# Optimization experiments

Hardware: AMD Instinct MI355X
Metric: run time of the kernel (lower is better)

The kernel has to match this reference:

```python
import jax, jax.numpy as jnp
import numpy as np

N, IN_DIM, OUT_DIM, HEADS = 2048, 512, 512, 8
HEAD_DIM = OUT_DIM // HEADS
NEG_SLOPE = 0.2


def setup_inputs() -> dict:
    key = jax.random.key(0)
    k1, k2, k3, k4 = jax.random.split(key, 4)
    x = jax.random.normal(k1, (N, IN_DIM), dtype=jnp.float32)
    adj = jax.random.randint(k2, (N, N), 0, 2, dtype=jnp.int32)
    W = jax.random.normal(k3, (IN_DIM, OUT_DIM), dtype=jnp.float32) * 0.02
    a = jax.random.normal(k4, (2 * HEAD_DIM,), dtype=jnp.float32) * 0.02
    return {"x": x, "adj": adj, "W": W, "a": a}


def reference(x, adj, W, a):
    # Wh: (N, H, Dh)
    Wh = (x @ W).reshape(N, HEADS, HEAD_DIM)
    # a . concat(Wh_i, Wh_j) == (Wh_i . a_src) + (Wh_j . a_dst) -- exact decomposition,
    # avoids materializing the (N, N, H, 2*Dh) concat tensor.
    a_src, a_dst = a[:HEAD_DIM], a[HEAD_DIM:]
    s_i = jnp.einsum('nhd,d->nh', Wh, a_src)  # contribution of dest node i
    s_j = jnp.einsum('nhd,d->nh', Wh, a_dst)  # contribution of source node j
    e = jax.nn.leaky_relu(s_i[:, None, :] + s_j[None, :, :], negative_slope=NEG_SLOPE)  # (N, N, H)
    mask = (adj > 0)[:, :, None]
    e = jnp.where(mask, e, jnp.float32(-jnp.inf))
    alpha = jax.nn.softmax(e, axis=1)  # softmax over source nodes j
    # out[i,h,:] = sum_j alpha[i,j,h] * Wh[j,h,:]   (dropout is identity at eval)
    out = jnp.einsum('ijh,jhd->ihd', alpha, Wh)
    return out.reshape(N, OUT_DIM)
```

## Files before the change

kernel.cpp:

```cpp
#include <hip/hip_runtime.h>
#include <hip/hip_bf16.h>

#define NN 2048
#define KD 512
#define ODIM 512
#define NHEAD 8
#define HD 64
#define NEG 0.2f

typedef float f32x4 __attribute__((ext_vector_type(4)));
typedef short bf16x8 __attribute__((ext_vector_type(8)));
typedef short bf16x4 __attribute__((ext_vector_type(4)));
typedef unsigned long long u64;
typedef unsigned int u32;

__device__ __forceinline__ short tob(float f) {
  __hip_bfloat16 h = __float2bfloat16(f);
  return *reinterpret_cast<short*>(&h);
}

__device__ __forceinline__ void gl_lds16(const void* g, void* l) {
  __builtin_amdgcn_global_load_lds(
      (const __attribute__((address_space(1))) u32*)g,
      (__attribute__((address_space(3))) u32*)l, 16, 0, 0);
}

__global__ __launch_bounds__(256) void prep(const float* __restrict__ W,
                                            const int* __restrict__ adj,
                                            __hip_bfloat16* __restrict__ WTb,
                                            unsigned short* __restrict__ bits) {
  const int b = blockIdx.x;
  const int t = threadIdx.x;
  if (b >= 64) {
    const int T = (b - 64) * 256 + t;
    const int row = T >> 7, g = T & 127;
    const int* p = adj + (size_t)row * NN + g * 16;
    u32 m = 0;
#pragma unroll
    for (int q = 0; q < 4; ++q) {
      const int4 v = *(const int4*)&p[q * 4];
      m |= (v.x > 0 ? 1u : 0u) << (q * 4);
      m |= (v.y > 0 ? 2u : 0u) << (q * 4);
      m |= (v.z > 0 ? 4u : 0u) << (q * 4);
      m |= (v.w > 0 ? 8u : 0u) << (q * 4);
    }
    bits[T] = (unsigned short)m;
    return;
  }
  __shared__ float tile[64][68];
  const int k0 = (b & 7) * 64, od0 = (b >> 3) * 64;
#pragma unroll
  for (int r = 0; r < 4; ++r) {
    const int flat = r * 256 + t;
    const int kk = flat >> 4, oq = (flat & 15) * 4;
    const float4 v = *(const float4*)&W[(size_t)(k0 + kk) * ODIM + od0 + oq];
    tile[kk][oq] = v.x;
    tile[kk][oq + 1] = v.y;
    tile[kk][oq + 2] = v.z;
    tile[kk][oq + 3] = v.w;
  }
  __syncthreads();
#pragma unroll
  for (int r = 0; r < 2; ++r) {
    const int flat = r * 256 + t;
    const int od = flat >> 3, kq = (flat & 7) * 8;
    bf16x8 o;
#pragma unroll
    for (int u = 0; u < 8; ++u) o[u] = tob(tile[kq + u][od]);
    *(bf16x8*)&WTb[(size_t)(od0 + od) * KD + k0 + kq] = o;
  }
}

__global__ __launch_bounds__(256) void gemm_fused(
    const float* __restrict__ X, const __hip_bfloat16* __restrict__ WTb,
    const float* __restrict__ a, short* __restrict__ WhF,
    float2* __restrict__ esrcp, u32* __restrict__ edstp) {
  __shared__ short As[64][72];
  __shared__ short Bs[64][72];
  const int t = threadIdx.x;
  const int lane = t & 63, w = t >> 6;
  const int col = lane & 15, kgrp = lane >> 4;
  const int bm = blockIdx.x * 64;
  const int h = blockIdx.y;

  const int am = t >> 2, ak = (t & 3) * 16;
  const int bn = t >> 2, bk = (t & 3) * 16;

  float4 xa[4];
  bf16x8 wb[2];
#pragma unroll
  for (int q = 0; q < 4; ++q)
    xa[q] = *(const float4*)&X[(size_t)(bm + am) * KD + ak + q * 4];
#pragma unroll
  for (int q = 0; q < 2; ++q)
    wb[q] = *(const bf16x8*)&WTb[(size_t)(h * 64 + bn) * KD + bk + q * 8];

  f32x4 acc[4] = {};

  for (int k0 = 0; k0 < KD; k0 += 64) {
#pragma unroll
    for (int q = 0; q < 2; ++q) {
      bf16x8 o;
#pragma unroll
      for (int u = 0; u < 4; ++u) {
        o[u] = tob(((const float*)&xa[q * 2])[u]);
        o[u + 4] = tob(((const float*)&xa[q * 2 + 1])[u]);
      }
      *(bf16x8*)&As[am][ak + q * 8] = o;
      *(bf16x8*)&Bs[bn][bk + q * 8] = wb[q];
    }
    __syncthreads();
    if (k0 + 64 < KD) {
      const int k1 = k0 + 64;
#pragma unroll
      for (int q = 0; q < 4; ++q)
        xa[q] = *(const float4*)&X[(size_t)(bm + am) * KD + k1 + ak + q * 4];
#pragma unroll
      for (int q = 0; q < 2; ++q)
        wb[q] = *(const bf16x8*)&WTb[(size_t)(h * 64 + bn) * KD + k1 + bk + q * 8];
    }
#pragma unroll
    for (int ks = 0; ks < 2; ++ks) {
      const bf16x8 af = *(const bf16x8*)&As[w * 16 + col][ks * 32 + kgrp * 8];
#pragma unroll
      for (int nt = 0; nt < 4; ++nt) {
        const bf16x8 bf = *(const bf16x8*)&Bs[nt * 16 + col][ks * 32 + kgrp * 8];
        acc[nt] = __builtin_amdgcn_mfma_f32_16x16x32_bf16(af, bf, acc[nt], 0, 0, 0);
      }
    }
    __syncthreads();
  }

  float asv[4], adv[4];
#pragma unroll
  for (int nt = 0; nt < 4; ++nt) {
    asv[nt] = a[nt * 16 + col];
    adv[nt] = a[64 + nt * 16 + col];
  }
  float ps[4], pd[4];
#pragma unroll
  for (int r = 0; r < 4; ++r) {
    float s1 = 0.f, s2 = 0.f;
#pragma unroll
    for (int nt = 0; nt < 4; ++nt) {
      s1 += acc[nt][r] * asv[nt];
      s2 += acc[nt][r] * adv[nt];
    }
    ps[r] = s1;
    pd[r] = s2;
  }
#pragma unroll
  for (int off = 1; off <= 8; off <<= 1) {
#pragma unroll
    for (int r = 0; r < 4; ++r) {
      ps[r] += __shfl_xor(ps[r], off);
      pd[r] += __shfl_xor(pd[r], off);
    }
  }
  {
    const size_t tbase = ((size_t)h * 32 + blockIdx.x) * 4096;
    const int lp = ((w & 1) * 2 + (kgrp >> 1)) * 16 + col;
    const int u0 = (kgrp & 1) * 4;
    const int slot_ks = w >> 1;
#pragma unroll
    for (int nt = 0; nt < 4; ++nt) {
      bf16x4 o;
#pragma unroll
      for (int r = 0; r < 4; ++r) o[r] = tob(acc[nt][r]);
      *(bf16x4*)&WhF[tbase + (size_t)(nt * 2 + slot_ks) * 512 + lp * 8 + u0] = o;
    }
  }
  if (col == 0) {
    const int mbase = bm + w * 16 + kgrp * 4;
#pragma unroll
    for (int r = 0; r < 4; ++r) {
      const int n = mbase + r;
      esrcp[h * NN + n] = make_float2(__expf(ps[r]), __expf(NEG * ps[r]));
      const u32 lo = (u32)(unsigned short)tob(__expf(pd[r]));
      const u32 hi = (u32)(unsigned short)tob(__expf(NEG * pd[r]));
      edstp[h * NN + n] = (hi << 16) | lo;
    }
  }
}

__global__ __launch_bounds__(256) void attn_mfma(
    const short* __restrict__ WhF, const unsigned char* __restrict__ adjbits,
    const float2* __restrict__ esrcp, const u32* __restrict__ edstp,
    float* __restrict__ out) {
  extern __shared__ __align__(16) char smem[];
  const int t = threadIdx.x;
  const int lane = t & 63;
  const int jq = t >> 6;
  const int col = lane & 15, kgrp = lane >> 4;
  const int h = blockIdx.y;
  const int i0 = blockIdx.x * 32;

  const short* tb = WhF + ((size_t)h * 32 + jq * 8) * 4096;
  const int jb = jq * 512;

  const float2 e0 = esrcp[h * NN + i0 + col];
  const float2 e1 = esrcp[h * NN + i0 + 16 + col];
  const float A0 = e0.x, C0 = e0.y, A1 = e1.x, C1 = e1.y;
  const unsigned char* ab0 = adjbits + (size_t)(i0 + col) * (NN / 8);
  const unsigned char* ab1 = adjbits + (size_t)(i0 + 16 + col) * (NN / 8);

  bf16x8 ones;
#pragma unroll
  for (int u = 0; u < 8; ++u) ones[u] = (short)0x3F80;

  f32x4 acc[2][4] = {};
  f32x4 accd[2] = {};

  uint4 bd[2][4];
  u64 aw[2][2];

  {
    short* sb = (short*)(smem + jq * 16384);
#pragma unroll
    for (int s = 0; s < 8; ++s) gl_lds16(tb + s * 512 + lane * 8, sb + s * 512);
    const int jj0 = jb + kgrp * 8;
    bd[0][0] = *(const uint4*)&edstp[h * NN + jj0];
    bd[0][1] = *(const uint4*)&edstp[h * NN + jj0 + 4];
    bd[0][2] = *(const uint4*)&edstp[h * NN + jj0 + 32];
    bd[0][3] = *(const uint4*)&edstp[h * NN + jj0 + 36];
    aw[0][0] = *(const u64*)(ab0 + (jb >> 3));
    aw[0][1] = *(const u64*)(ab1 + (jb >> 3));
  }

#pragma unroll
  for (int tt = 0; tt < 8; ++tt) {
    const int cur = tt & 1, nxt = cur ^ 1;
    if (tt < 7) {
      const short* g = tb + (size_t)(tt + 1) * 4096;
      short* sb = (short*)(smem + jq * 16384 + nxt * 8192);
#pragma unroll
      for (int s = 0; s < 8; ++s)
        gl_lds16(g + s * 512 + lane * 8, sb + s * 512);
      const int j1 = jb + (tt + 1) * 64;
      const int jj1 = j1 + kgrp * 8;
      bd[nxt][0] = *(const uint4*)&edstp[h * NN + jj1];
      bd[nxt][1] = *(const uint4*)&edstp[h * NN + jj1 + 4];
      bd[nxt][2] = *(const uint4*)&edstp[h * NN + jj1 + 32];
      bd[nxt][3] = *(const uint4*)&edstp[h * NN + jj1 + 36];
      aw[nxt][0] = *(const u64*)(ab0 + (j1 >> 3));
      aw[nxt][1] = *(const u64*)(ab1 + (j1 >> 3));
      asm volatile("s_waitcnt vmcnt(14)" ::: "memory");
    } else {
      asm volatile("s_waitcnt vmcnt(0)" ::: "memory");
    }
    __builtin_amdgcn_sched_barrier(0);

    bf16x8 af0[2], af1[2];
#pragma unroll
    for (int ks = 0; ks < 2; ++ks) {
      const u32 mb0 = (u32)(aw[cur][0] >> ((ks * 4 + kgrp) * 8)) & 0xffu;
      const u32 mb1 = (u32)(aw[cur][1] >> ((ks * 4 + kgrp) * 8)) & 0xffu;
      const uint4 q0 = bd[cur][ks * 2];
      const uint4 q1 = bd[cur][ks * 2 + 1];
      const u32 uw[8] = {q0.x, q0.y, q0.z, q0.w, q1.x, q1.y, q1.z, q1.w};
#pragma unroll
      for (int u2 = 0; u2 < 8; ++u2) {
        const float B = __uint_as_float(uw[u2] << 16);
        const float D = __uint_as_float(uw[u2] & 0xffff0000u);
        float p0 = fmaxf(A0 * B, C0 * D);
        float p1 = fmaxf(A1 * B, C1 * D);
        p0 = ((mb0 >> u2) & 1u) ? p0 : 0.f;
        p1 = ((mb1 >> u2) & 1u) ? p1 : 0.f;
        af0[ks][u2] = tob(p0);
        af1[ks][u2] = tob(p1);
      }
    }

    const short* scur = (const short*)(smem + jq * 16384 + cur * 8192);
    accd[0] = __builtin_amdgcn_mfma_f32_16x16x32_bf16(af0[0], ones, accd[0], 0, 0, 0);
    accd[0] = __builtin_amdgcn_mfma_f32_16x16x32_bf16(af0[1], ones, accd[0], 0, 0, 0);
    accd[1] = __builtin_amdgcn_mfma_f32_16x16x32_bf16(af1[0], ones, accd[1], 0, 0, 0);
    accd[1] = __builtin_amdgcn_mfma_f32_16x16x32_bf16(af1[1], ones, accd[1], 0, 0, 0);
#pragma unroll
    for (int nt = 0; nt < 4; ++nt) {
      const bf16x8 b0 = *(const bf16x8*)&scur[(nt * 2 + 0) * 512 + lane * 8];
      const bf16x8 b1 = *(const bf16x8*)&scur[(nt * 2 + 1) * 512 + lane * 8];
      acc[0][nt] = __builtin_amdgcn_mfma_f32_16x16x32_bf16(af0[0], b0, acc[0][nt], 0, 0, 0);
      acc[1][nt] = __builtin_amdgcn_mfma_f32_16x16x32_bf16(af1[0], b0, acc[1][nt], 0, 0, 0);
      acc[0][nt] = __builtin_amdgcn_mfma_f32_16x16x32_bf16(af0[1], b1, acc[0][nt], 0, 0, 0);
      acc[1][nt] = __builtin_amdgcn_mfma_f32_16x16x32_bf16(af1[1], b1, acc[1][nt], 0, 0, 0);
    }
  }

  __syncthreads();
  float* red = (float*)smem;
  float* rw = red + (size_t)jq * 32 * 66;
#pragma unroll
  for (int mt = 0; mt < 2; ++mt) {
#pragma unroll
    for (int nt = 0; nt < 4; ++nt)
#pragma unroll
      for (int r = 0; r < 4; ++r)
        rw[(mt * 16 + kgrp * 4 + r) * 66 + nt * 16 + col] = acc[mt][nt][r];
    if (col == 0) {
#pragma unroll
      for (int r = 0; r < 4; ++r)
        rw[(mt * 16 + kgrp * 4 + r) * 66 + 64] = accd[mt][r];
    }
  }
  __syncthreads();

  const int d = t & 63, rl = t >> 6;
#pragma unroll
  for (int rr = 0; rr < 8; ++rr) {
    const int row = rr * 4 + rl;
    float v = 0.f, dd = 0.f;
#pragma unroll
    for (int q = 0; q < 4; ++q) {
      v += red[((size_t)q * 32 + row) * 66 + d];
      dd += red[((size_t)q * 32 + row) * 66 + 64];
    }
    out[(size_t)(i0 + row) * ODIM + h * HD + d] = v / dd;
  }
}

extern "C" void kernel_launch(void* const* d_in, const int* in_sizes, int n_in,
                              void* d_out, int out_size, void* d_ws,
                              size_t ws_size, hipStream_t stream) {
  const float* x = (const float*)d_in[0];
  const int* adj = (const int*)d_in[1];
  const float* W = (const float*)d_in[2];
  const float* a = (const float*)d_in[3];
  float* out = (float*)d_out;

  char* ws = (char*)d_ws;
  short* WhF = (short*)ws;
  __hip_bfloat16* WTb = (__hip_bfloat16*)(ws + (2 << 20));
  unsigned short* bits =
      (unsigned short*)(ws + (2 << 20) + (512 << 10));
  float2* esrcp = (float2*)(ws + (3 << 20));
  u32* edstp = (u32*)(ws + (3 << 20) + (128 << 10));

  prep<<<1088, 256, 0, stream>>>(W, adj, WTb, bits);
  gemm_fused<<<dim3(32, 8), 256, 0, stream>>>(x, WTb, a, WhF, esrcp, edstp);
  attn_mfma<<<dim3(64, 8), 256, 65536, stream>>>(
      WhF, (const unsigned char*)bits, esrcp, edstp, out);
}
```

Baseline: 36.18 us.

## Pre-swizzle X and W into MFMA fragment layout; stage attention metadata via LDS

The prep kernel now converts X to bf16 and writes both X and W in MFMA-fragment order. This lets the GEMM drop its LDS staging and syncthreads and load fragments straight from global memory. In the attention kernel, the edst values and adjacency bits are loaded asynchronously into LDS with global_load_lds instead of into registers, and the MFMA section is wrapped in s_setprio. The aim is fewer registers and less synchronization in both kernels, at the cost of an extra full bf16 copy of X written and read through memory.

Result: slower. 37.31 us (+3.1%).

```diff
diff --git a/kernel.cpp b/kernel.cpp
--- a/kernel.cpp
+++ b/kernel.cpp
@@ -24,15 +24,24 @@
       (const __attribute__((address_space(1))) u32*)g,
       (__attribute__((address_space(3))) u32*)l, 16, 0, 0);
 }
-
-__global__ __launch_bounds__(256) void prep(const float* __restrict__ W,
+__device__ __forceinline__ void gl_lds4(const void* g, void* l) {
+  __builtin_amdgcn_global_load_lds(
+      (const __attribute__((address_space(1))) u32*)g,
+      (__attribute__((address_space(3))) u32*)l, 4, 0, 0);
+}
+
+__global__ __launch_bounds__(256) void prep(const float* __restrict__ X,
+                                            const float* __restrict__ W,
                                             const int* __restrict__ adj,
-                                            __hip_bfloat16* __restrict__ WTb,
+                                            short* __restrict__ Xf,
+                                            short* __restrict__ Bf,
                                             unsigned short* __restrict__ bits) {
+  __shared__ float sbuf[16 * 516];
   const int b = blockIdx.x;
   const int t = threadIdx.x;
-  if (b >= 64) {
-    const int T = (b - 64) * 256 + t;
+
+  if (b < 1024) {
+    const int T = b * 256 + t;
     const int row = T >> 7, g = T & 127;
     const int* p = adj + (size_t)row * NN + g * 16;
     u32 m = 0;
@@ -47,88 +56,81 @@
     bits[T] = (unsigned short)m;
     return;
   }
-  __shared__ float tile[64][68];
-  const int k0 = (b & 7) * 64, od0 = (b >> 3) * 64;
-#pragma unroll
-  for (int r = 0; r < 4; ++r) {
-    const int flat = r * 256 + t;
-    const int kk = flat >> 4, oq = (flat & 15) * 4;
-    const float4 v = *(const float4*)&W[(size_t)(k0 + kk) * ODIM + od0 + oq];
-    tile[kk][oq] = v.x;
-    tile[kk][oq + 1] = v.y;
-    tile[kk][oq + 2] = v.z;
-    tile[kk][oq + 3] = v.w;
+
+  if (b < 1024 + 128) {
+    const int xb = b - 1024;
+#pragma unroll
+    for (int q = 0; q < 8; ++q) {
+      const int flat = q * 256 + t;
+      const int row = flat >> 7, c4 = flat & 127;
+      const float4 v = *(const float4*)&X[(size_t)(xb * 16 + row) * KD + c4 * 4];
+      *(float4*)&sbuf[row * 516 + c4 * 4] = v;
+    }
+    __syncthreads();
+#pragma unroll
+    for (int c = 0; c < 4; ++c) {
+      const int s = c * 256 + t;
+      const int ks = s >> 6, l = s & 63;
+      const int col = l & 15, kg = (l >> 4) & 3;
+      const int k0 = ks * 32 + kg * 8;
+      bf16x8 o;
+#pragma unroll
+      for (int u = 0; u < 8; ++u) o[u] = tob(sbuf[col * 516 + k0 + u]);
+      *(bf16x8*)&Xf[((size_t)xb * 1024 + s) * 8] = o;
+    }
+    return;
+  }
+
+  const int b2 = b - 1152;
+  const int kb = b2 & 7, h = b2 >> 3;
+  const int k0 = kb * 64;
+#pragma unroll
+  for (int q = 0; q < 4; ++q) {
+    const int flat = q * 256 + t;
+    const int kk = flat >> 4, o4 = (flat & 15) * 4;
+    const float4 v = *(const float4*)&W[(size_t)(k0 + kk) * ODIM + h * 64 + o4];
+    *(float4*)&sbuf[kk * 68 + o4] = v;
   }
   __syncthreads();
 #pragma unroll
-  for (int r = 0; r < 2; ++r) {
-    const int flat = r * 256 + t;
-    const int od = flat >> 3, kq = (flat & 7) * 8;
+  for (int c = 0; c < 2; ++c) {
+    const int s = c * 256 + t;
+    const int ksl = s >> 8, nt = (s >> 6) & 3, l = s & 63;
+    const int col = l & 15, kg = (l >> 4) & 3;
+    const int kloc = ksl * 32 + kg * 8;
+    const int od = nt * 16 + col;
     bf16x8 o;
 #pragma unroll
-    for (int u = 0; u < 8; ++u) o[u] = tob(tile[kq + u][od]);
-    *(bf16x8*)&WTb[(size_t)(od0 + od) * KD + k0 + kq] = o;
+    for (int u = 0; u < 8; ++u) o[u] = tob(sbuf[(kloc + u) * 68 + od]);
+    const size_t off = (((size_t)(h * 4 + nt) * 16 + kb * 2 + ksl) * 64 + l) * 8;
+    *(bf16x8*)&Bf[off] = o;
   }
 }
 
 __global__ __launch_bounds__(256) void gemm_fused(
-    const float* __restrict__ X, const __hip_bfloat16* __restrict__ WTb,
+    const short* __restrict__ Xf, const short* __restrict__ Bf,
     const float* __restrict__ a, short* __restrict__ WhF,
     float2* __restrict__ esrcp, u32* __restrict__ edstp) {
-  __shared__ short As[64][72];
-  __shared__ short Bs[64][72];
   const int t = threadIdx.x;
   const int lane = t & 63, w = t >> 6;
   const int col = lane & 15, kgrp = lane >> 4;
   const int bm = blockIdx.x * 64;
   const int h = blockIdx.y;
-
-  const int am = t >> 2, ak = (t & 3) * 16;
-  const int bn = t >> 2, bk = (t & 3) * 16;
-
-  float4 xa[4];
-  bf16x8 wb[2];
-#pragma unroll
-  for (int q = 0; q < 4; ++q)
-    xa[q] = *(const float4*)&X[(size_t)(bm + am) * KD + ak + q * 4];
-#pragma unroll
-  for (int q = 0; q < 2; ++q)
-    wb[q] = *(const bf16x8*)&WTb[(size_t)(h * 64 + bn) * KD + bk + q * 8];
+  const int mt = blockIdx.x * 4 + w;
+
+  const short* ax = Xf + (size_t)mt * 8192;
+  const short* bx = Bf + (size_t)h * 32768;
 
   f32x4 acc[4] = {};
 
-  for (int k0 = 0; k0 < KD; k0 += 64) {
-#pragma unroll
-    for (int q = 0; q < 2; ++q) {
-      bf16x8 o;
-#pragma unroll
-      for (int u = 0; u < 4; ++u) {
-        o[u] = tob(((const float*)&xa[q * 2])[u]);
-        o[u + 4] = tob(((const float*)&xa[q * 2 + 1])[u]);
-      }
-      *(bf16x8*)&As[am][ak + q * 8] = o;
-      *(bf16x8*)&Bs[bn][bk + q * 8] = wb[q];
-    }
-    __syncthreads();
-    if (k0 + 64 < KD) {
-      const int k1 = k0 + 64;
-#pragma unroll
-      for (int q = 0; q < 4; ++q)
-        xa[q] = *(const float4*)&X[(size_t)(bm + am) * KD + k1 + ak + q * 4];
-#pragma unroll
-      for (int q = 0; q < 2; ++q)
-        wb[q] = *(const bf16x8*)&WTb[(size_t)(h * 64 + bn) * KD + k1 + bk + q * 8];
-    }
-#pragma unroll
-    for (int ks = 0; ks < 2; ++ks) {
-      const bf16x8 af = *(const bf16x8*)&As[w * 16 + col][ks * 32 + kgrp * 8];
-#pragma unroll
-      for (int nt = 0; nt < 4; ++nt) {
-        const bf16x8 bf = *(const bf16x8*)&Bs[nt * 16 + col][ks * 32 + kgrp * 8];
-        acc[nt] = __builtin_amdgcn_mfma_f32_16x16x32_bf16(af, bf, acc[nt], 0, 0, 0);
-      }
-    }
-    __syncthreads();
+#pragma unroll
+  for (int ks = 0; ks < 16; ++ks) {
+    const bf16x8 af = *(const bf16x8*)&ax[(ks * 64 + lane) * 8];
+#pragma unroll
+    for (int nt = 0; nt < 4; ++nt) {
+      const bf16x8 bf = *(const bf16x8*)&bx[((nt * 16 + ks) * 64 + lane) * 8];
+      acc[nt] = __builtin_amdgcn_mfma_f32_16x16x32_bf16(af, bf, acc[nt], 0, 0, 0);
+    }
   }
 
   float asv[4], adv[4];
@@ -194,15 +196,15 @@
   const int col = lane & 15, kgrp = lane >> 4;
   const int h = blockIdx.y;
   const int i0 = blockIdx.x * 32;
+  char* wbase = smem + jq * 17408;
 
   const short* tb = WhF + ((size_t)h * 32 + jq * 8) * 4096;
   const int jb = jq * 512;
+  const int jboff = jb >> 3;
 
   const float2 e0 = esrcp[h * NN + i0 + col];
   const float2 e1 = esrcp[h * NN + i0 + 16 + col];
   const float A0 = e0.x, C0 = e0.y, A1 = e1.x, C1 = e1.y;
-  const unsigned char* ab0 = adjbits + (size_t)(i0 + col) * (NN / 8);
-  const unsigned char* ab1 = adjbits + (size_t)(i0 + 16 + col) * (NN / 8);
 
   bf16x8 ones;
 #pragma unroll
@@ -211,52 +213,45 @@
   f32x4 acc[2][4] = {};
   f32x4 accd[2] = {};
 
-  uint4 bd[2][4];
-  u64 aw[2][2];
-
   {
-    short* sb = (short*)(smem + jq * 16384);
-#pragma unroll
-    for (int s = 0; s < 8; ++s) gl_lds16(tb + s * 512 + lane * 8, sb + s * 512);
-    const int jj0 = jb + kgrp * 8;
-    bd[0][0] = *(const uint4*)&edstp[h * NN + jj0];
-    bd[0][1] = *(const uint4*)&edstp[h * NN + jj0 + 4];
-    bd[0][2] = *(const uint4*)&edstp[h * NN + jj0 + 32];
-    bd[0][3] = *(const uint4*)&edstp[h * NN + jj0 + 36];
-    aw[0][0] = *(const u64*)(ab0 + (jb >> 3));
-    aw[0][1] = *(const u64*)(ab1 + (jb >> 3));
+    char* bb = wbase;
+#pragma unroll
+    for (int s = 0; s < 8; ++s)
+      gl_lds16(tb + s * 512 + lane * 8, bb + s * 1024);
+    gl_lds4(edstp + h * NN + jb + lane, bb + 8192);
+    gl_lds4(adjbits + (size_t)(i0 + (lane >> 1)) * 256 + jboff + (lane & 1) * 4,
+            bb + 8448);
   }
 
 #pragma unroll
   for (int tt = 0; tt < 8; ++tt) {
-    const int cur = tt & 1, nxt = cur ^ 1;
+    char* bcur = wbase + (tt & 1) * 8704;
+    char* bnxt = wbase + ((tt + 1) & 1) * 8704;
     if (tt < 7) {
       const short* g = tb + (size_t)(tt + 1) * 4096;
-      short* sb = (short*)(smem + jq * 16384 + nxt * 8192);
 #pragma unroll
       for (int s = 0; s < 8; ++s)
-        gl_lds16(g + s * 512 + lane * 8, sb + s * 512);
-      const int j1 = jb + (tt + 1) * 64;
-      const int jj1 = j1 + kgrp * 8;
-      bd[nxt][0] = *(const uint4*)&edstp[h * NN + jj1];
-      bd[nxt][1] = *(const uint4*)&edstp[h * NN + jj1 + 4];
-      bd[nxt][2] = *(const uint4*)&edstp[h * NN + jj1 + 32];
-      bd[nxt][3] = *(const uint4*)&edstp[h * NN + jj1 + 36];
-      aw[nxt][0] = *(const u64*)(ab0 + (j1 >> 3));
-      aw[nxt][1] = *(const u64*)(ab1 + (j1 >> 3));
-      asm volatile("s_waitcnt vmcnt(14)" ::: "memory");
+        gl_lds16(g + s * 512 + lane * 8, bnxt + s * 1024);
+      gl_lds4(edstp + h * NN + jb + (tt + 1) * 64 + lane, bnxt + 8192);
+      gl_lds4(adjbits + (size_t)(i0 + (lane >> 1)) * 256 + jboff +
+                  (tt + 1) * 8 + (lane & 1) * 4,
+              bnxt + 8448);
+      asm volatile("s_waitcnt vmcnt(10)" ::: "memory");
     } else {
       asm volatile("s_waitcnt vmcnt(0)" ::: "memory");
     }
     __builtin_amdgcn_sched_barrier(0);
 
+    const u32* elds = (const u32*)(bcur + 8192);
+    const u64 m0 = *(const u64*)(bcur + 8448 + col * 8);
+    const u64 m1 = *(const u64*)(bcur + 8448 + 128 + col * 8);
     bf16x8 af0[2], af1[2];
 #pragma unroll
     for (int ks = 0; ks < 2; ++ks) {
-      const u32 mb0 = (u32)(aw[cur][0] >> ((ks * 4 + kgrp) * 8)) & 0xffu;
-      const u32 mb1 = (u32)(aw[cur][1] >> ((ks * 4 + kgrp) * 8)) & 0xffu;
-      const uint4 q0 = bd[cur][ks * 2];
-      const uint4 q1 = bd[cur][ks * 2 + 1];
+      const uint4 q0 = *(const uint4*)&elds[ks * 32 + kgrp * 8];
+      const uint4 q1 = *(const uint4*)&elds[ks * 32 + kgrp * 8 + 4];
+      const u32 mb0 = (u32)(m0 >> ((ks * 4 + kgrp) * 8)) & 0xffu;
+      const u32 mb1 = (u32)(m1 >> ((ks * 4 + kgrp) * 8)) & 0xffu;
       const u32 uw[8] = {q0.x, q0.y, q0.z, q0.w, q1.x, q1.y, q1.z, q1.w};
 #pragma unroll
       for (int u2 = 0; u2 < 8; ++u2) {
@@ -271,20 +266,22 @@
       }
     }
 
-    const short* scur = (const short*)(smem + jq * 16384 + cur * 8192);
+    const short* sb = (const short*)bcur;
+    __builtin_amdgcn_s_setprio(1);
     accd[0] = __builtin_amdgcn_mfma_f32_16x16x32_bf16(af0[0], ones, accd[0], 0, 0, 0);
     accd[0] = __builtin_amdgcn_mfma_f32_16x16x32_bf16(af0[1], ones, accd[0], 0, 0, 0);
     accd[1] = __builtin_amdgcn_mfma_f32_16x16x32_bf16(af1[0], ones, accd[1], 0, 0, 0);
     accd[1] = __builtin_amdgcn_mfma_f32_16x16x32_bf16(af1[1], ones, accd[1], 0, 0, 0);
 #pragma unroll
     for (int nt = 0; nt < 4; ++nt) {
-      const bf16x8 b0 = *(const bf16x8*)&scur[(nt * 2 + 0) * 512 + lane * 8];
-      const bf16x8 b1 = *(const bf16x8*)&scur[(nt * 2 + 1) * 512 + lane * 8];
+      const bf16x8 b0 = *(const bf16x8*)&sb[(nt * 2 + 0) * 512 + lane * 8];
+      const bf16x8 b1 = *(const bf16x8*)&sb[(nt * 2 + 1) * 512 + lane * 8];
       acc[0][nt] = __builtin_amdgcn_mfma_f32_16x16x32_bf16(af0[0], b0, acc[0][nt], 0, 0, 0);
       acc[1][nt] = __builtin_amdgcn_mfma_f32_16x16x32_bf16(af1[0], b0, acc[1][nt], 0, 0, 0);
       acc[0][nt] = __builtin_amdgcn_mfma_f32_16x16x32_bf16(af0[1], b1, acc[0][nt], 0, 0, 0);
       acc[1][nt] = __builtin_amdgcn_mfma_f32_16x16x32_bf16(af1[1], b1, acc[1][nt], 0, 0, 0);
     }
+    __builtin_amdgcn_s_setprio(0);
   }
 
   __syncthreads();
@@ -330,14 +327,15 @@
 
   char* ws = (char*)d_ws;
   short* WhF = (short*)ws;
-  __hip_bfloat16* WTb = (__hip_bfloat16*)(ws + (2 << 20));
+  short* Xf = (short*)(ws + (2 << 20));
+  short* Bf = (short*)(ws + (4 << 20));
   unsigned short* bits =
-      (unsigned short*)(ws + (2 << 20) + (512 << 10));
-  float2* esrcp = (float2*)(ws + (3 << 20));
-  u32* edstp = (u32*)(ws + (3 << 20) + (128 << 10));
-
-  prep<<<1088, 256, 0, stream>>>(W, adj, WTb, bits);
-  gemm_fused<<<dim3(32, 8), 256, 0, stream>>>(x, WTb, a, WhF, esrcp, edstp);
-  attn_mfma<<<dim3(64, 8), 256, 65536, stream>>>(
+      (unsigned short*)(ws + (4 << 20) + (512 << 10));
+  float2* esrcp = (float2*)(ws + (5 << 20));
+  u32* edstp = (u32*)(ws + (5 << 20) + (128 << 10));
+
+  prep<<<1216, 256, 0, stream>>>(x, W, adj, Xf, Bf, bits);
+  gemm_fused<<<dim3(32, 8), 256, 0, stream>>>(Xf, Bf, a, WhF, esrcp, edstp);
+  attn_mfma<<<dim3(64, 8), 256, 69632, stream>>>(
       WhF, (const unsigned char*)bits, esrcp, edstp, out);
 }
```
